# Kernel tuning notes

Measured on AMD Instinct MI355X. Metric: run time of the kernel, lower is better.

The kernel has to match this reference:

```python
import jax, jax.numpy as jnp
import numpy as np
from jax import lax

B, N, G, K, D = 32, 32768, 64, 32, 384
EPS = 1e-5


def _fps(xyz, npoint):
    # Farthest point sampling; deterministic start at index 0 (original uses randint).
    b, n, _ = xyz.shape
    def step(carry, _):
        distance, farthest = carry
        centroid = jnp.take_along_axis(xyz, farthest[:, None, None], axis=1)  # (B,1,3)
        dist = jnp.sum((xyz - centroid) ** 2, axis=-1)                        # (B,N)
        distance = jnp.minimum(distance, dist)
        new_far = jnp.argmax(distance, axis=-1)
        return (distance, new_far), farthest
    init = (jnp.full((b, n), 1e10, xyz.dtype), jnp.zeros((b,), jnp.int32))
    _, cents = lax.scan(step, init, None, length=npoint)  # (npoint, B)
    return cents.T  # (B, npoint)


def _bn(h, g, bta, m, v):
    # inference-mode BatchNorm over channel (last) dim
    return (h - m) * (g * lax.rsqrt(v + EPS)) + bta


def setup_inputs() -> dict:
    key = jax.random.key(0)
    ks = jax.random.split(key, 5)
    xyz = jax.random.normal(ks[0], (B, N, 3), jnp.float32)
    features = jax.random.normal(ks[1], (B, N, 3), jnp.float32)
    w1 = jax.random.normal(ks[2], (64, 6), jnp.float32) * 0.1
    w2 = jax.random.normal(ks[3], (128, 64), jnp.float32) * 0.1
    w3 = jax.random.normal(ks[4], (D, 128), jnp.float32) * 0.1
    def bn(c):
        return jnp.ones((c,), jnp.float32), jnp.zeros((c,), jnp.float32), jnp.zeros((c,), jnp.float32), jnp.ones((c,), jnp.float32)
    g1, b1, m1, v1 = bn(64)
    g2, b2, m2, v2 = bn(128)
    g3, b3, m3, v3 = bn(D)
    return dict(xyz=xyz, features=features, w1=w1, g1=g1, b1=b1, m1=m1, v1=v1,
                w2=w2, g2=g2, b2=b2, m2=m2, v2=v2, w3=w3, g3=g3, b3=b3, m3=m3, v3=v3)


def reference(xyz, features, w1, g1, b1, m1, v1, w2, g2, b2, m2, v2, w3, g3, b3, m3, v3):
    fps_idx = _fps(xyz, G)                                           # (B,G)
    center = jnp.take_along_axis(xyz, fps_idx[:, :, None], axis=1)   # (B,G,3)
    # KNN via squared distances (same ordering as torch.cdist euclidean)
    xn2 = jnp.sum(xyz * xyz, axis=-1)                                # (B,N)
    cn2 = jnp.sum(center * center, axis=-1)                          # (B,G)
    d2 = cn2[:, :, None] + xn2[:, None, :] - 2.0 * jnp.einsum('bgc,bnc->bgn', center, xyz)
    _, knn_idx = lax.top_k(-d2, K)                                   # (B,G,K)
    gx = jax.vmap(lambda x, i: x[i])(xyz, knn_idx)                   # (B,G,K,3)
    gf = jax.vmap(lambda f, i: f[i])(features, knn_idx)              # (B,G,K,3)
    h = jnp.concatenate([gx - center[:, :, None, :], gf], axis=-1)   # (B,G,K,6)
    h = jax.nn.relu(_bn(jnp.einsum('bgkc,oc->bgko', h, w1), g1, b1, m1, v1))
    h = jax.nn.relu(_bn(jnp.einsum('bgkc,oc->bgko', h, w2), g2, b2, m2, v2))
    h = _bn(jnp.einsum('bgkc,oc->bgko', h, w3), g3, b3, m3, v3)      # (B,G,K,D)
    patch = jnp.max(h, axis=2)                                       # (B,G,D) adaptive max pool
    return center, patch
```

## Files before the change

### kernel.cpp

```cpp
#include <hip/hip_runtime.h>
#include <hip/hip_bf16.h>

#define BB 32
#define NN 32768
#define GG 64
#define KK 32
#define DD 384
#define EPSF 1e-5f
#define FPS_NBLK 8
#define FPS_SL   (NN/FPS_NBLK)

typedef __attribute__((ext_vector_type(8))) short short8;
typedef __attribute__((ext_vector_type(4))) float f32x4;

__device__ __forceinline__ float rn_add(float a, float b){ return __fadd_rn(a,b); }
__device__ __forceinline__ float rn_sub(float a, float b){ return __fsub_rn(a,b); }
__device__ __forceinline__ float rn_mul(float a, float b){ return __fmul_rn(a,b); }

__device__ __forceinline__ unsigned fkey(float d){
  unsigned u = __float_as_uint(d);
  return (u & 0x80000000u) ? ~u : (u | 0x80000000u);
}

__device__ __forceinline__ unsigned short f2bf(float f){
  unsigned u = __float_as_uint(f);
  unsigned r = (u + 0x7FFFu + ((u >> 16) & 1u)) >> 16;
  return (unsigned short)r;
}

#define REP8(X) X(0) X(1) X(2) X(3) X(4) X(5) X(6) X(7)

__device__ float g_center[BB*GG*3];
__device__ int   g_knn[BB*GG*KK];
__device__ float g_w1t[6*64];
__device__ float g_b1[64];
__device__ float g_b2[128];
__device__ float g_b3[384];
__device__ __align__(16) unsigned short g_w2f[8*2*64*8];
__device__ __align__(16) unsigned short g_w3f[24*4*64*8];
__device__ float g_X[BB*NN];
__device__ float g_Y[BB*NN];
__device__ float g_Z[BB*NN];
__device__ float g_N2[BB*NN];
__device__ unsigned long long g_part[BB*FPS_NBLK*GG];

__global__ __launch_bounds__(256) void k_soa(const float* __restrict__ xyz){
  int tid = blockIdx.x * blockDim.x + threadIdx.x;
  int b = tid >> 15;
  int p = tid & (NN - 1);
  const float* s = xyz + (size_t)b*NN*3 + (size_t)p*3;
  float x = s[0], y = s[1], z = s[2];
  g_X[tid] = x;
  g_Y[tid] = y;
  g_Z[tid] = z;
  g_N2[tid] = rn_add(rn_add(rn_mul(x,x), rn_mul(y,y)), rn_mul(z,z));
}

__global__ __launch_bounds__(256) void k_zero(void){
  int tid = blockIdx.x * blockDim.x + threadIdx.x;
  if (tid < BB*FPS_NBLK*GG) g_part[tid] = 0ull;
}

__global__ void k_prep(const float* __restrict__ w1, const float* __restrict__ g1, const float* __restrict__ b1, const float* __restrict__ m1, const float* __restrict__ v1,
                       const float* __restrict__ w2, const float* __restrict__ g2, const float* __restrict__ b2, const float* __restrict__ m2, const float* __restrict__ v2,
                       const float* __restrict__ w3, const float* __restrict__ g3, const float* __restrict__ b3, const float* __restrict__ m3, const float* __restrict__ v3){
  int tid = blockIdx.x * blockDim.x + threadIdx.x;
  int nt  = gridDim.x * blockDim.x;
  for (int e = tid; e < 64*6; e += nt){
    int c = e >> 6, o = e & 63;
    float s = g1[o] * rsqrtf(v1[o] + EPSF);
    g_w1t[e] = w1[o*6 + c] * s;
  }
  for (int o = tid; o < 64; o += nt){
    float s = g1[o] * rsqrtf(v1[o] + EPSF);
    g_b1[o] = b1[o] - m1[o]*s;
  }
  for (int o = tid; o < 128; o += nt){
    float s = g2[o] * rsqrtf(v2[o] + EPSF);
    g_b2[o] = b2[o] - m2[o]*s;
  }
  for (int o = tid; o < 384; o += nt){
    float s = g3[o] * rsqrtf(v3[o] + EPSF);
    g_b3[o] = b3[o] - m3[o]*s;
  }
  for (int idx = tid; idx < 8192; idx += nt){
    int e  = idx & 7;
    int l  = (idx >> 3) & 63;
    int kt = (idx >> 9) & 1;
    int ct = idx >> 10;
    int j  = ct*16 + (l & 15);
    int k  = kt*32 + ((l >> 4) << 3) + e;
    float s = g2[j] * rsqrtf(v2[j] + EPSF);
    g_w2f[idx] = f2bf(w2[j*64 + k] * s);
  }
  for (int idx = tid; idx < 49152; idx += nt){
    int e  = idx & 7;
    int l  = (idx >> 3) & 63;
    int kt = (idx >> 9) & 3;
    int ct = idx >> 11;
    int j  = ct*16 + (l & 15);
    int k  = kt*32 + ((l >> 4) << 3) + e;
    float s = g3[j] * rsqrtf(v3[j] + EPSF);
    g_w3f[idx] = f2bf(w3[j*128 + k] * s);
  }
}

__global__ __launch_bounds__(512)
void k_fps(float* __restrict__ outCenter){
  const int blk = blockIdx.x;
  const int b   = blk & 31;
  const int sub = blk >> 5;
  const int t   = threadIdx.x;
  const int wv  = t >> 6, ln = t & 63;
  const int base = sub * FPS_SL;
  const float* Xb = g_X + (size_t)b*NN;
  const float* Yb = g_Y + (size_t)b*NN;
  const float* Zb = g_Z + (size_t)b*NN;

  __shared__ float sx[FPS_SL], sy[FPS_SL], szz[FPS_SL];
  __shared__ unsigned long long skey[8];
  __shared__ int s_far;

  #pragma unroll
  for (int i = 0; i < 8; ++i){
    int p = (i << 9) + t;
    sx[p]  = Xb[base + p];
    sy[p]  = Yb[base + p];
    szz[p] = Zb[base + p];
  }
  __syncthreads();

#define DD_DECL(i) float dd##i = 1e10f;
  REP8(DD_DECL)
#undef DD_DECL

  int far = 0;
  for (int it = 0; ; ++it){
    if (sub == 0 && t == 0){
      float cx = Xb[far], cy = Yb[far], cz = Zb[far];
      float* cw = g_center  + (size_t)(b*GG + it)*3;
      float* co = outCenter + (size_t)(b*GG + it)*3;
      cw[0] = cx; cw[1] = cy; cw[2] = cz;
      co[0] = cx; co[1] = cy; co[2] = cz;
    }
    if (it == GG - 1) break;

    float cx = Xb[far], cy = Yb[far], cz = Zb[far];
    unsigned long long bk = 0ull;
#define DD_UPD(i) { \
    int p = (i << 9) + t; \
    float dx = rn_sub(sx[p], cx); \
    float dy = rn_sub(sy[p], cy); \
    float dz = rn_sub(szz[p], cz); \
    float s_ = rn_add(rn_add(rn_mul(dx,dx), rn_mul(dy,dy)), rn_mul(dz,dz)); \
    float d_ = fminf(dd##i, s_); \
    dd##i = d_; \
    unsigned long long k_ = ((unsigned long long)fkey(d_) << 32) \
                          | (unsigned)(0xFFFFFFFFu - (unsigned)(base + p)); \
    if (k_ > bk) bk = k_; }
    REP8(DD_UPD)
#undef DD_UPD

    #pragma unroll
    for (int off = 32; off >= 1; off >>= 1){
      unsigned long long o = (unsigned long long)__shfl_xor((long long)bk, off);
      if (o > bk) bk = o;
    }
    if (ln == 0) skey[wv] = bk;
    __syncthreads();
    if (wv == 0){
      unsigned long long m = (ln < 8) ? skey[ln] : 0ull;
      #pragma unroll
      for (int off = 1; off <= 4; off <<= 1){
        unsigned long long o = (unsigned long long)__shfl_xor((long long)m, off);
        if (o > m) m = o;
      }
      if (ln == 0)
        __hip_atomic_store(&g_part[(((b << 3) + sub) << 6) + it], m,
                           __ATOMIC_RELAXED, __HIP_MEMORY_SCOPE_AGENT);
      unsigned long long k = 0ull;
      if (ln < 8){
        unsigned long long* p = &g_part[(((b << 3) + ln) << 6) + it];
        do {
          k = __hip_atomic_load(p, __ATOMIC_RELAXED, __HIP_MEMORY_SCOPE_AGENT);
        } while (k == 0ull);
      }
      #pragma unroll
      for (int off = 1; off <= 4; off <<= 1){
        unsigned long long o = (unsigned long long)__shfl_xor((long long)k, off);
        if (o > k) k = o;
      }
      if (ln == 0) s_far = (int)(0xFFFFFFFFu - (unsigned)(k & 0xFFFFFFFFu));
    }
    __syncthreads();
    far = s_far;
  }
}

__global__ __launch_bounds__(256) void k_knn(void){
  const int j  = blockIdx.x;
  const int b  = (j & 7) + ((j >> 7) << 3);
  const int g0 = ((j >> 3) & 15) << 2;
  const int t  = threadIdx.x;
  const int w  = t >> 6;
  const int ln = t & 63;
  const float4* X4 = (const float4*)(g_X  + (size_t)b*NN);
  const float4* Y4 = (const float4*)(g_Y  + (size_t)b*NN);
  const float4* Z4 = (const float4*)(g_Z  + (size_t)b*NN);
  const float4* N4 = (const float4*)(g_N2 + (size_t)b*NN);

  __shared__ float sC[4][4];
  __shared__ unsigned sE[4][64];
  __shared__ unsigned sTk[4];
  __shared__ unsigned long long cand[4][512];
  __shared__ int cnt[4];

  if (t < 4){
    const float* cp = g_center + (size_t)(b*GG + g0 + t)*3;
    float x = cp[0], y = cp[1], z = cp[2];
    sC[0][t] = x; sC[1][t] = y; sC[2][t] = z;
    sC[3][t] = rn_add(rn_add(rn_mul(x,x), rn_mul(y,y)), rn_mul(z,z));
    cnt[t] = 0;
  }
  __syncthreads();

  float cx[4], cy[4], cz[4], cn[4];
  #pragma unroll
  for (int c = 0; c < 4; ++c){
    cx[c] = sC[0][c]; cy[c] = sC[1][c]; cz[c] = sC[2][c]; cn[c] = sC[3][c];
  }

  float e0[4], e1[4];
  #pragma unroll
  for (int c = 0; c < 4; ++c){ e0[c] = INFINITY; e1[c] = INFINITY; }
  #pragma unroll 2
  for (int s = 0; s < 32; ++s){
    int q = (s << 8) + t;
    float4 x = X4[q], y = Y4[q], z = Z4[q], n = N4[q];
    #pragma unroll
    for (int c = 0; c < 4; ++c){
      #define P1C(comp) { \
        float e = rn_add(rn_add(rn_mul(cx[c],x.comp), rn_mul(cy[c],y.comp)), rn_mul(cz[c],z.comp)); \
        float d = rn_sub(rn_add(cn[c], n.comp), rn_add(e,e)); \
        float nm2 = fminf(e1[c], fmaxf(e0[c], d)); \
        e0[c] = fminf(e0[c], d); \
        e1[c] = nm2; }
      P1C(x) P1C(y) P1C(z) P1C(w)
      #undef P1C
    }
  }

  #pragma unroll
  for (int c = 0; c < 4; ++c){
    unsigned v = fkey(e1[c]);
    #pragma unroll
    for (int k = 2; k <= 64; k <<= 1){
      #pragma unroll
      for (int jj = k >> 1; jj > 0; jj >>= 1){
        unsigned o = (unsigned)__shfl_xor((int)v, jj);
        bool keepmin = (((ln & k) == 0) == ((ln & jj) == 0));
        unsigned mn = o < v ? o : v;
        unsigned mx = o < v ? v : o;
        v = keepmin ? mn : mx;
      }
    }
    if (ln < 16) sE[c][w*16 + ln] = v;
  }
  __syncthreads();

  {
    unsigned v = sE[w][ln];
    #pragma unroll
    for (int k = 2; k <= 64; k <<= 1){
      #pragma unroll
      for (int jj = k >> 1; jj > 0; jj >>= 1){
        unsigned o = (unsigned)__shfl_xor((int)v, jj);
        bool keepmin = (((ln & k) == 0) == ((ln & jj) == 0));
        unsigned mn = o < v ? o : v;
        unsigned mx = o < v ? v : o;
        v = keepmin ? mn : mx;
      }
    }
    unsigned T = (unsigned)__shfl((int)v, 15);
    if (ln == 0) sTk[w] = T;
  }
  __syncthreads();

  unsigned Tr[4];
  #pragma unroll
  for (int c = 0; c < 4; ++c) Tr[c] = sTk[c];

  #pragma unroll 2
  for (int s = 0; s < 32; ++s){
    int q = (s << 8) + t;
    float4 x = X4[q], y = Y4[q], z = Z4[q], n = N4[q];
    #pragma unroll
    for (int c = 0; c < 4; ++c){
      #define P2C(comp, kk) { \
        float e = rn_add(rn_add(rn_mul(cx[c],x.comp), rn_mul(cy[c],y.comp)), rn_mul(cz[c],z.comp)); \
        float d = rn_sub(rn_add(cn[c], n.comp), rn_add(e,e)); \
        unsigned fk = fkey(d); \
        if (fk <= Tr[c]){ \
          int p = atomicAdd(&cnt[c], 1); \
          if (p < 512) \
            cand[c][p] = ((unsigned long long)fk << 32) | (unsigned)((q<<2)+kk); } }
      P2C(x,0) P2C(y,1) P2C(z,2) P2C(w,3)
      #undef P2C
    }
  }
  __syncthreads();

  {
    int C = cnt[w]; if (C > 512) C = 512;
    int* kout = g_knn + (size_t)(b*GG + g0 + w)*KK;
    if (C <= 64){
      unsigned long long kk = (ln < C) ? cand[w][ln] : ~0ull;
      #pragma unroll
      for (int k = 2; k <= 64; k <<= 1){
        #pragma unroll
        for (int jj = k >> 1; jj > 0; jj >>= 1){
          unsigned long long o = (unsigned long long)__shfl_xor((long long)kk, jj);
          bool keepmin = (((ln & k) == 0) == ((ln & jj) == 0));
          unsigned long long mn = o < kk ? o : kk;
          unsigned long long mx = o < kk ? kk : o;
          kk = keepmin ? mn : mx;
        }
      }
      if (ln < KK) kout[ln] = (int)(kk & 0xffffffffu);
    } else {
      unsigned long long md[8];
      #pragma unroll
      for (int jj = 0; jj < 8; ++jj){
        int e = ln + (jj << 6);
        md[jj] = (e < C) ? cand[w][e] : ~0ull;
      }
      for (int r = 0; r < KK; ++r){
        unsigned long long bk = md[0];
        #pragma unroll
        for (int jj = 1; jj < 8; ++jj) if (md[jj] < bk) bk = md[jj];
        #pragma unroll
        for (int off = 32; off >= 1; off >>= 1){
          unsigned long long o = (unsigned long long)__shfl_xor((long long)bk, off);
          if (o < bk) bk = o;
        }
        #pragma unroll
        for (int jj = 0; jj < 8; ++jj) if (md[jj] == bk) md[jj] = ~0ull;
        if (ln == 0) kout[r] = (int)(bk & 0xffffffffu);
      }
    }
  }
}

__global__ __launch_bounds__(256) void k_mlp(const float* __restrict__ xyz,
                                             const float* __restrict__ feat,
                                             float* __restrict__ outPatch){
  const int bg = blockIdx.x;
  const int b  = bg >> 6;
  const int t  = threadIdx.x;
  const int w  = t >> 6;
  const int ln = t & 63;
  const float* xb = xyz  + (size_t)b*NN*3;
  const float* fb = feat + (size_t)b*NN*3;

  __shared__ float h0[KK][8];
  __shared__ __align__(16) unsigned short h1b[KK][72];
  __shared__ __align__(16) unsigned short h2b[KK][136];

  if (t < KK){
    int idx = g_knn[(size_t)bg*KK + t] & (NN - 1);
    const float* cp = g_center + (size_t)bg*3;
    h0[t][0] = rn_sub(xb[idx*3+0], cp[0]);
    h0[t][1] = rn_sub(xb[idx*3+1], cp[1]);
    h0[t][2] = rn_sub(xb[idx*3+2], cp[2]);
    h0[t][3] = fb[idx*3+0];
    h0[t][4] = fb[idx*3+1];
    h0[t][5] = fb[idx*3+2];
  }
  __syncthreads();

  {
    int p = t >> 3, ob = (t & 7) * 8;
    float acc[8];
    #pragma unroll
    for (int j = 0; j < 8; ++j) acc[j] = g_b1[ob + j];
    #pragma unroll
    for (int c = 0; c < 6; ++c){
      float a = h0[p][c];
      const float4* wr = (const float4*)(g_w1t + c*64 + ob);
      float4 wa = wr[0], wb = wr[1];
      acc[0] = fmaf(a, wa.x, acc[0]); acc[1] = fmaf(a, wa.y, acc[1]);
      acc[2] = fmaf(a, wa.z, acc[2]); acc[3] = fmaf(a, wa.w, acc[3]);
      acc[4] = fmaf(a, wb.x, acc[4]); acc[5] = fmaf(a, wb.y, acc[5]);
      acc[6] = fmaf(a, wb.z, acc[6]); acc[7] = fmaf(a, wb.w, acc[7]);
    }
    short8 v;
    #pragma unroll
    for (int j = 0; j < 8; ++j) v[j] = (short)f2bf(fmaxf(acc[j], 0.f));
    *reinterpret_cast<short8*>(&h1b[p][ob]) = v;
  }
  __syncthreads();

  {
    f32x4 a00 = {0,0,0,0}, a01 = {0,0,0,0}, a10 = {0,0,0,0}, a11 = {0,0,0,0};
    const int g8 = (ln >> 4) << 3;
    #pragma unroll
    for (int kk = 0; kk < 2; ++kk){
      short8 A0 = *reinterpret_cast<const short8*>(&h1b[(ln & 15)][kk*32 + g8]);
      short8 A1 = *reinterpret_cast<const short8*>(&h1b[16 + (ln & 15)][kk*32 + g8]);
      short8 B0 = *reinterpret_cast<const short8*>(&g_w2f[(((2*w+0)*2 + kk)*64 + ln)*8]);
      short8 B1 = *reinterpret_cast<const short8*>(&g_w2f[(((2*w+1)*2 + kk)*64 + ln)*8]);
      a00 = __builtin_amdgcn_mfma_f32_16x16x32_bf16(A0, B0, a00, 0, 0, 0);
      a01 = __builtin_amdgcn_mfma_f32_16x16x32_bf16(A1, B0, a01, 0, 0, 0);
      a10 = __builtin_amdgcn_mfma_f32_16x16x32_bf16(A0, B1, a10, 0, 0, 0);
      a11 = __builtin_amdgcn_mfma_f32_16x16x32_bf16(A1, B1, a11, 0, 0, 0);
    }
    int col0 = (2*w)*16 + (ln & 15);
    int col1 = col0 + 16;
    float bz0 = g_b2[col0], bz1 = g_b2[col1];
    int r0 = (ln >> 4) << 2;
    #pragma unroll
    for (int r = 0; r < 4; ++r){
      h2b[r0 + r][col0]      = f2bf(fmaxf(a00[r] + bz0, 0.f));
      h2b[16 + r0 + r][col0] = f2bf(fmaxf(a01[r] + bz0, 0.f));
      h2b[r0 + r][col1]      = f2bf(fmaxf(a10[r] + bz1, 0.f));
      h2b[16 + r0 + r][col1] = f2bf(fmaxf(a11[r] + bz1, 0.f));
    }
  }
  __syncthreads();

  {
    f32x4 acc3[6][2];
    #pragma unroll
    for (int ci = 0; ci < 6; ++ci){
      acc3[ci][0] = (f32x4){0,0,0,0};
      acc3[ci][1] = (f32x4){0,0,0,0};
    }
    const int g8 = (ln >> 4) << 3;
    #pragma unroll
    for (int kk = 0; kk < 4; ++kk){
      short8 A0 = *reinterpret_cast<const short8*>(&h2b[(ln & 15)][kk*32 + g8]);
      short8 A1 = *reinterpret_cast<const short8*>(&h2b[16 + (ln & 15)][kk*32 + g8]);
      #pragma unroll
      for (int ci = 0; ci < 6; ++ci){
        int ct = w*6 + ci;
        short8 B = *reinterpret_cast<const short8*>(&g_w3f[((ct*4 + kk)*64 + ln)*8]);
        acc3[ci][0] = __builtin_amdgcn_mfma_f32_16x16x32_bf16(A0, B, acc3[ci][0], 0, 0, 0);
        acc3[ci][1] = __builtin_amdgcn_mfma_f32_16x16x32_bf16(A1, B, acc3[ci][1], 0, 0, 0);
      }
    }
    #pragma unroll
    for (int ci = 0; ci < 6; ++ci){
      float m = acc3[ci][0][0];
      #pragma unroll
      for (int r = 1; r < 4; ++r) m = fmaxf(m, acc3[ci][0][r]);
      #pragma unroll
      for (int r = 0; r < 4; ++r) m = fmaxf(m, acc3[ci][1][r]);
      m = fmaxf(m, __shfl_xor(m, 16));
      m = fmaxf(m, __shfl_xor(m, 32));
      if (ln < 16){
        int col = (w*6 + ci)*16 + ln;
        outPatch[(size_t)bg*DD + col] = m + g_b3[col];
      }
    }
  }
}

extern "C" void kernel_launch(void* const* d_in, const int* in_sizes, int n_in,
                              void* d_out, int out_size, void* d_ws, size_t ws_size,
                              hipStream_t stream){
  (void)in_sizes; (void)n_in; (void)out_size; (void)d_ws; (void)ws_size;
  const float* xyz  = (const float*)d_in[0];
  const float* feat = (const float*)d_in[1];
  const float* w1 = (const float*)d_in[2];
  const float* g1 = (const float*)d_in[3];
  const float* b1 = (const float*)d_in[4];
  const float* m1 = (const float*)d_in[5];
  const float* v1 = (const float*)d_in[6];
  const float* w2 = (const float*)d_in[7];
  const float* g2 = (const float*)d_in[8];
  const float* b2 = (const float*)d_in[9];
  const float* m2 = (const float*)d_in[10];
  const float* v2 = (const float*)d_in[11];
  const float* w3 = (const float*)d_in[12];
  const float* g3 = (const float*)d_in[13];
  const float* b3 = (const float*)d_in[14];
  const float* m3 = (const float*)d_in[15];
  const float* v3 = (const float*)d_in[16];
  float* out = (float*)d_out;

  k_prep<<<64, 256, 0, stream>>>(w1,g1,b1,m1,v1, w2,g2,b2,m2,v2, w3,g3,b3,m3,v3);
  k_soa<<<(BB*NN)/256, 256, 0, stream>>>(xyz);
  k_zero<<<64, 256, 0, stream>>>();
  k_fps<<<BB*FPS_NBLK, 512, 0, stream>>>(out);
  k_knn<<<512, 256, 0, stream>>>();
  k_mlp<<<BB*GG, 256, 0, stream>>>(xyz, feat, out + (size_t)BB*GG*3);
}
```

Before: 246.9 us.

## Publish winning centroid coordinates with tagged double-buffered slots in FPS exchange

Each FPS block now publishes its local winner key together with that point's x/y/z coordinates, taken from shared memory, into a tagged, double-buffered global slot. The winning coordinates are then shuffled across lanes, so no block has to reload the centroid from global memory after the cross-block reduction. Iteration tags replace the per-iteration zeroed partial array, which shrinks the zero-init kernel. This removes a dependent global load from each of the 63 serial iterations. The cost is more atomic stores and polls per iteration, and a key encoding that assumes the point index fits in 15 bits.

```diff
diff --git a/kernel.cpp b/kernel.cpp
--- a/kernel.cpp
+++ b/kernel.cpp
@@ -42,7 +42,7 @@
 __device__ float g_Y[BB*NN];
 __device__ float g_Z[BB*NN];
 __device__ float g_N2[BB*NN];
-__device__ unsigned long long g_part[BB*FPS_NBLK*GG];
+__device__ unsigned long long g_slot[BB*FPS_NBLK*2*8];
 
 __global__ __launch_bounds__(256) void k_soa(const float* __restrict__ xyz){
   int tid = blockIdx.x * blockDim.x + threadIdx.x;
@@ -58,7 +58,7 @@
 
 __global__ __launch_bounds__(256) void k_zero(void){
   int tid = blockIdx.x * blockDim.x + threadIdx.x;
-  if (tid < BB*FPS_NBLK*GG) g_part[tid] = 0ull;
+  if (tid < BB*FPS_NBLK*2*8) g_slot[tid] = 0ull;
 }
 
 __global__ void k_prep(const float* __restrict__ w1, const float* __restrict__ g1, const float* __restrict__ b1, const float* __restrict__ m1, const float* __restrict__ v1,
@@ -119,7 +119,7 @@
 
   __shared__ float sx[FPS_SL], sy[FPS_SL], szz[FPS_SL];
   __shared__ unsigned long long skey[8];
-  __shared__ int s_far;
+  __shared__ float s_cx, s_cy, s_cz;
 
   #pragma unroll
   for (int i = 0; i < 8; ++i){
@@ -134,10 +134,10 @@
   REP8(DD_DECL)
 #undef DD_DECL
 
-  int far = 0;
+  float cx = Xb[0], cy = Yb[0], cz = Zb[0];
+
   for (int it = 0; ; ++it){
     if (sub == 0 && t == 0){
-      float cx = Xb[far], cy = Yb[far], cz = Zb[far];
       float* cw = g_center  + (size_t)(b*GG + it)*3;
       float* co = outCenter + (size_t)(b*GG + it)*3;
       cw[0] = cx; cw[1] = cy; cw[2] = cz;
@@ -145,7 +145,7 @@
     }
     if (it == GG - 1) break;
 
-    float cx = Xb[far], cy = Yb[far], cz = Zb[far];
+    const unsigned tagv = (unsigned)(it + 1);
     unsigned long long bk = 0ull;
 #define DD_UPD(i) { \
     int p = (i << 9) + t; \
@@ -156,7 +156,7 @@
     float d_ = fminf(dd##i, s_); \
     dd##i = d_; \
     unsigned long long k_ = ((unsigned long long)fkey(d_) << 32) \
-                          | (unsigned)(0xFFFFFFFFu - (unsigned)(base + p)); \
+                          | (tagv << 15) | (unsigned)(32767 - (base + p)); \
     if (k_ > bk) bk = k_; }
     REP8(DD_UPD)
 #undef DD_UPD
@@ -175,25 +175,51 @@
         unsigned long long o = (unsigned long long)__shfl_xor((long long)m, off);
         if (o > m) m = o;
       }
-      if (ln == 0)
-        __hip_atomic_store(&g_part[(((b << 3) + sub) << 6) + it], m,
-                           __ATOMIC_RELAXED, __HIP_MEMORY_SCOPE_AGENT);
-      unsigned long long k = 0ull;
-      if (ln < 8){
-        unsigned long long* p = &g_part[(((b << 3) + ln) << 6) + it];
-        do {
-          k = __hip_atomic_load(p, __ATOMIC_RELAXED, __HIP_MEMORY_SCOPE_AGENT);
-        } while (k == 0ull);
-      }
+      if (ln == 0){
+        int pl = (32767 - (int)(m & 0x7FFFu)) - base;
+        unsigned long long* S =
+            &g_slot[((((b << 3) + sub) << 1) + (it & 1)) << 3];
+        unsigned long long xv = ((unsigned long long)tagv << 32) | __float_as_uint(sx[pl]);
+        unsigned long long yv = ((unsigned long long)tagv << 32) | __float_as_uint(sy[pl]);
+        unsigned long long zv = ((unsigned long long)tagv << 32) | __float_as_uint(szz[pl]);
+        __hip_atomic_store(S + 0, m,  __ATOMIC_RELAXED, __HIP_MEMORY_SCOPE_AGENT);
+        __hip_atomic_store(S + 1, xv, __ATOMIC_RELAXED, __HIP_MEMORY_SCOPE_AGENT);
+        __hip_atomic_store(S + 2, yv, __ATOMIC_RELAXED, __HIP_MEMORY_SCOPE_AGENT);
+        __hip_atomic_store(S + 3, zv, __ATOMIC_RELAXED, __HIP_MEMORY_SCOPE_AGENT);
+      }
+      unsigned long long v = 0ull;
+      const int grp = ln >> 3, sb = ln & 7;
+      if (ln < 32){
+        unsigned long long* P =
+            &g_slot[(((((b << 3) + sb) << 1) + (it & 1)) << 3) + grp];
+        if (grp == 0){
+          do { v = __hip_atomic_load(P, __ATOMIC_RELAXED, __HIP_MEMORY_SCOPE_AGENT); }
+          while ((((unsigned)v) >> 15) != tagv);
+        } else {
+          do { v = __hip_atomic_load(P, __ATOMIC_RELAXED, __HIP_MEMORY_SCOPE_AGENT); }
+          while ((unsigned)(v >> 32) != tagv);
+        }
+      }
+      unsigned long long k = (ln < 8) ? v : 0ull;
+      int ws = sb;
       #pragma unroll
       for (int off = 1; off <= 4; off <<= 1){
-        unsigned long long o = (unsigned long long)__shfl_xor((long long)k, off);
-        if (o > k) k = o;
-      }
-      if (ln == 0) s_far = (int)(0xFFFFFFFFu - (unsigned)(k & 0xFFFFFFFFu));
+        unsigned long long ok = (unsigned long long)__shfl_xor((long long)k, off);
+        int ows = __shfl_xor(ws, off);
+        if (ok > k){ k = ok; ws = ows; }
+      }
+      ws = __shfl(ws, 0);
+      unsigned long long vx = (unsigned long long)__shfl((long long)v,  8 + ws);
+      unsigned long long vy = (unsigned long long)__shfl((long long)v, 16 + ws);
+      unsigned long long vz = (unsigned long long)__shfl((long long)v, 24 + ws);
+      if (ln == 0){
+        s_cx = __uint_as_float((unsigned)(vx & 0xFFFFFFFFu));
+        s_cy = __uint_as_float((unsigned)(vy & 0xFFFFFFFFu));
+        s_cz = __uint_as_float((unsigned)(vz & 0xFFFFFFFFu));
+      }
     }
     __syncthreads();
-    far = s_far;
+    cx = s_cx; cy = s_cy; cz = s_cz;
   }
 }
 
@@ -490,7 +516,7 @@
 
   k_prep<<<64, 256, 0, stream>>>(w1,g1,b1,m1,v1, w2,g2,b2,m2,v2, w3,g3,b3,m3,v3);
   k_soa<<<(BB*NN)/256, 256, 0, stream>>>(xyz);
-  k_zero<<<64, 256, 0, stream>>>();
+  k_zero<<<2, 256, 0, stream>>>();
   k_fps<<<BB*FPS_NBLK, 512, 0, stream>>>(out);
   k_knn<<<512, 256, 0, stream>>>();
   k_mlp<<<BB*GG, 256, 0, stream>>>(xyz, feat, out + (size_t)BB*GG*3);
```

After: 279.5 us. 1.13x slower.
